# Kernel tuning notes

Hardware: AMD Instinct MI355X
Metric: run time of the kernel (lower is better)

The kernel has to match this reference:

```python
import jax, jax.numpy as jnp
import numpy as np

H = 256
W = 256
N = 10000
CHUNK = 500  # N must be divisible by CHUNK
CHOL_BOUND = np.array([0.5, 0.0, 0.5], dtype=np.float32)  # cholesky_bound buffer


def setup_inputs() -> dict:
    key = jax.random.key(0)
    k1, k2, k3 = jax.random.split(key, 3)
    xyz = jax.random.normal(k1, (N, 2), dtype=jnp.float32)          # atanh-space positions
    cholesky = jax.random.uniform(k2, (N, 3), dtype=jnp.float32)    # lower-tri elems (pre-bound)
    colors = jax.random.normal(k3, (N, 3), dtype=jnp.float32)       # _colors (used raw)
    opacity = jnp.ones((N, 1), dtype=jnp.float32)                   # _opacity buffer
    scale_factor = jnp.asarray(1.0, dtype=jnp.float32)
    shift_factor = jnp.asarray(0.0, dtype=jnp.float32)
    return {"xyz": xyz, "cholesky": cholesky, "colors": colors,
            "opacity": opacity, "scale_factor": scale_factor, "shift_factor": shift_factor}


def _render(xyz, cholesky, colors, opacity, scale_factor, shift_factor):
    # --- project_gaussians_2d ---
    means = jnp.tanh(xyz)                                   # map to (-1, 1)
    cx = 0.5 * W * (means[:, 0] + 1.0)                      # pixel-space centers (N,)
    cy = 0.5 * H * (means[:, 1] + 1.0)
    L = cholesky + jnp.asarray(CHOL_BOUND)                  # get_cholesky_elements
    cov_xx = L[:, 0] * L[:, 0]
    cov_xy = L[:, 0] * L[:, 1]
    cov_yy = L[:, 1] * L[:, 1] + L[:, 2] * L[:, 2]
    det = cov_xx * cov_yy - cov_xy * cov_xy
    conic_a = cov_yy / det                                  # inverse covariance (conic)
    conic_b = -cov_xy / det
    conic_c = cov_xx / det
    op = opacity[:, 0]

    px = jnp.arange(W, dtype=jnp.float32)[None, :]          # (1, W) pixel x coords
    py = jnp.arange(H, dtype=jnp.float32)[:, None]          # (H, 1) pixel y coords

    def resh(v):
        return v.reshape((N // CHUNK, CHUNK) + v.shape[1:])

    stacked = jax.tree.map(resh, (cx, cy, conic_a, conic_b, conic_c, op, colors))

    # --- rasterize_gaussians_sum: out[h,w,:] = sum_n alpha_n(h,w) * color_n ---
    def body(acc, xs):
        cxc, cyc, ac, bc, cc, oc, colc = xs
        dx = cxc[:, None, None] - px[None]                  # (C, 1, W)
        dy = cyc[:, None, None] - py[None]                  # (C, H, 1)
        sigma = (0.5 * (ac[:, None, None] * dx * dx + cc[:, None, None] * dy * dy)
                 + bc[:, None, None] * (dx * dy))           # (C, H, W)
        alpha = oc[:, None, None] * jnp.exp(-sigma)
        alpha = jnp.where((sigma >= 0.0) & (alpha >= 1.0 / 255.0),
                          jnp.minimum(alpha, 0.999), 0.0)
        acc = acc + jnp.einsum('nhw,nc->hwc', alpha, colc)
        return acc, None

    img, _ = jax.lax.scan(body, jnp.zeros((H, W, 3), dtype=jnp.float32), stacked)
    img = img * scale_factor + shift_factor
    return jnp.transpose(img, (2, 0, 1))                    # (3, H, W)


def reference(xyz, cholesky, colors, opacity, scale_factor, shift_factor):
    return _render(xyz, cholesky, colors, opacity, scale_factor, shift_factor)
```

## Files before the change

### kernel.cpp

```cpp
#include <hip/hip_runtime.h>


#define IMG_H 256
#define IMG_W 256
#define TILE 8
#define TPX 32
#define NTILES 1024
#define CAP 512

__global__ __launch_bounds__(256) void prep_kernel(
    const float* __restrict__ xyz,
    const float* __restrict__ chol,
    const float* __restrict__ colors,
    const float* __restrict__ opacity,
    int N,
    unsigned int* __restrict__ bbox,
    float4* __restrict__ params)
{
    const int n = blockIdx.x * 256 + threadIdx.x;
    if (n >= N) return;

    const float mx = tanhf(xyz[2 * n + 0]);
    const float my = tanhf(xyz[2 * n + 1]);
    const float cx = 0.5f * IMG_W * (mx + 1.0f);
    const float cy = 0.5f * IMG_H * (my + 1.0f);

    const float L0 = chol[3 * n + 0] + 0.5f;
    const float L1 = chol[3 * n + 1];
    const float L2 = chol[3 * n + 2] + 0.5f;
    const float cov_xx = L0 * L0;
    const float cov_xy = L0 * L1;
    const float cov_yy = L1 * L1 + L2 * L2;
    const float det = cov_xx * cov_yy - cov_xy * cov_xy;

    params[3 * n + 0] = make_float4(cx, cy, cov_yy / det, -cov_xy / det);
    params[3 * n + 1] = make_float4(cov_xx / det, opacity[n],
                                    colors[3 * n + 0], colors[3 * n + 1]);
    params[3 * n + 2] = make_float4(colors[3 * n + 2], 0.0f, 0.0f, 0.0f);

    const float smax = logf(255.0f * opacity[n]);
    unsigned int packed = 0xFFFFFFFFu;
    if (smax > 0.0f) {
        const float rx = sqrtf(2.0f * smax * cov_xx) + 1.0f;
        const float ry = sqrtf(2.0f * smax * cov_yy) + 1.0f;
        const int x0 = max(0, (int)floorf(cx - rx));
        const int x1 = min(IMG_W - 1, (int)ceilf(cx + rx));
        const int y0 = max(0, (int)floorf(cy - ry));
        const int y1 = min(IMG_H - 1, (int)ceilf(cy + ry));
        if (x0 <= x1 && y0 <= y1) {
            packed = (unsigned int)(x0 >> 3) | ((unsigned int)(x1 >> 3) << 5) |
                     ((unsigned int)(y0 >> 3) << 10) | ((unsigned int)(y1 >> 3) << 15);
        }
    }
    bbox[n] = packed;
}

__global__ __launch_bounds__(256) void render_kernel(
    const unsigned int* __restrict__ bbox,
    const float4* __restrict__ params,
    const float* __restrict__ scale,
    const float* __restrict__ shift,
    int N,
    float* __restrict__ out)
{
    const int tile = blockIdx.x;
    const int tx = tile & (TPX - 1);
    const int ty = tile >> 5;
    const int wave = threadIdx.x >> 6;
    const int lane = threadIdx.x & 63;
    const int p = lane;
    const float px = (float)(tx * TILE + (p & (TILE - 1)));
    const float py = (float)(ty * TILE + (p >> 3));

    __shared__ int lcnt;
    __shared__ int lidx[CAP];
    __shared__ float4 sh[3 * 256];
    __shared__ float red[3][256];

    if (threadIdx.x == 0) lcnt = 0;
    __syncthreads();

    const unsigned int txu = (unsigned int)tx;
    const unsigned int tyu = (unsigned int)ty;
    for (int i = threadIdx.x; i < N; i += 256) {
        const unsigned int b = bbox[i];
        const bool match = ((b & 31u) <= txu) && (txu <= ((b >> 5) & 31u)) &&
                           (((b >> 10) & 31u) <= tyu) && (tyu <= ((b >> 15) & 31u));
        const unsigned long long mask = __ballot(match);
        if (match) {
            const int leader = __ffsll((long long)mask) - 1;
            const int pos = __popcll(mask & ((1ull << lane) - 1ull));
            int basep = 0;
            if (lane == leader) basep = atomicAdd(&lcnt, __popcll(mask));
            basep = __shfl(basep, leader);
            const int slot = basep + pos;
            if (slot < CAP) lidx[slot] = i;
        }
    }
    __syncthreads();
    const int cnt = min(lcnt, CAP);

    float accr = 0.0f, accg = 0.0f, accb = 0.0f;

    for (int base = 0; base < cnt; base += 256) {
        const int m = min(256, cnt - base);
        if (threadIdx.x < m) {
            const int n = lidx[base + threadIdx.x];
            sh[3 * threadIdx.x + 0] = params[3 * n + 0];
            sh[3 * threadIdx.x + 1] = params[3 * n + 1];
            sh[3 * threadIdx.x + 2] = params[3 * n + 2];
        }
        __syncthreads();
        for (int j = wave; j < m; j += 4) {
            const float4 p0 = sh[3 * j + 0];
            const float4 p1 = sh[3 * j + 1];
            const float c2v = sh[3 * j + 2].x;
            const float dx = p0.x - px;
            const float dy = p0.y - py;
            const float sigma =
                0.5f * (p0.z * dx * dx + p1.x * dy * dy) + p0.w * (dx * dy);
            float alpha = p1.y * __expf(-sigma);
            if (sigma >= 0.0f && alpha >= (1.0f / 255.0f)) {
                alpha = fminf(alpha, 0.999f);
                accr = fmaf(alpha, p1.z, accr);
                accg = fmaf(alpha, p1.w, accg);
                accb = fmaf(alpha, c2v, accb);
            }
        }
        __syncthreads();
    }

    red[0][threadIdx.x] = accr;
    red[1][threadIdx.x] = accg;
    red[2][threadIdx.x] = accb;
    __syncthreads();

    if (threadIdx.x < 192) {
        const int c = threadIdx.x >> 6;
        const int q = threadIdx.x & 63;
        const float sum = red[c][q] + red[c][q + 64] + red[c][q + 128] + red[c][q + 192];
        const int pix = (ty * TILE + (q >> 3)) * IMG_W + tx * TILE + (q & (TILE - 1));
        out[c * IMG_H * IMG_W + pix] = fmaf(sum, scale[0], shift[0]);
    }
}

extern "C" void kernel_launch(void* const* d_in, const int* in_sizes, int n_in,
                              void* d_out, int out_size, void* d_ws, size_t ws_size,
                              hipStream_t stream) {
    const float* xyz     = (const float*)d_in[0];
    const float* chol    = (const float*)d_in[1];
    const float* colors  = (const float*)d_in[2];
    const float* opacity = (const float*)d_in[3];
    const float* scale   = (const float*)d_in[4];
    const float* shift   = (const float*)d_in[5];
    float* out = (float*)d_out;

    const int N = in_sizes[3];

    unsigned int* bbox = (unsigned int*)d_ws;
    float4* params = (float4*)((char*)d_ws + ((N * 4 + 15) & ~15));

    prep_kernel<<<(N + 255) / 256, 256, 0, stream>>>(
        xyz, chol, colors, opacity, N, bbox, params);
    render_kernel<<<NTILES, 256, 0, stream>>>(bbox, params, scale, shift, N, out);
}
```

Measured before the change: 83.89 us.

## Replace atomic ballot compaction with per-thread private lists and block prefix scan

The per-tile culling pass no longer uses a ballot plus LDS atomic per match. Each thread now buffers up to 16 matching indices in shared memory, then a block-wide Hillis-Steele scan computes offsets for an ordered compaction. The change also permutes the tile-to-block mapping, splits the parameter staging into float4 pairs plus a scalar array, and unrolls the inner loop. It adds many barriers during the scan, hardcodes a 40-iteration loop (assumes N ≤ 10240), and silently drops matches beyond 16 per thread.

```diff
diff --git a/kernel.cpp b/kernel.cpp
--- a/kernel.cpp
+++ b/kernel.cpp
@@ -7,6 +7,7 @@
 #define TPX 32
 #define NTILES 1024
 #define CAP 512
+#define PRIV 16
 
 __global__ __launch_bounds__(256) void prep_kernel(
     const float* __restrict__ xyz,
@@ -33,13 +34,14 @@
     const float cov_yy = L1 * L1 + L2 * L2;
     const float det = cov_xx * cov_yy - cov_xy * cov_xy;
 
+    const float op = opacity[n];
     params[3 * n + 0] = make_float4(cx, cy, cov_yy / det, -cov_xy / det);
-    params[3 * n + 1] = make_float4(cov_xx / det, opacity[n],
+    params[3 * n + 1] = make_float4(cov_xx / det, op,
                                     colors[3 * n + 0], colors[3 * n + 1]);
     params[3 * n + 2] = make_float4(colors[3 * n + 2], 0.0f, 0.0f, 0.0f);
 
-    const float smax = logf(255.0f * opacity[n]);
-    unsigned int packed = 0xFFFFFFFFu;
+    const float smax = logf(255.0f * op);
+    unsigned int packed = 31u | (31u << 10);
     if (smax > 0.0f) {
         const float rx = sqrtf(2.0f * smax * cov_xx) + 1.0f;
         const float ry = sqrtf(2.0f * smax * cov_yy) + 1.0f;
@@ -63,42 +65,51 @@
     int N,
     float* __restrict__ out)
 {
-    const int tile = blockIdx.x;
+    const int tile = (blockIdx.x * 389) & (NTILES - 1);
     const int tx = tile & (TPX - 1);
     const int ty = tile >> 5;
     const int wave = threadIdx.x >> 6;
-    const int lane = threadIdx.x & 63;
-    const int p = lane;
+    const int p = threadIdx.x & 63;
     const float px = (float)(tx * TILE + (p & (TILE - 1)));
     const float py = (float)(ty * TILE + (p >> 3));
 
-    __shared__ int lcnt;
+    __shared__ int lpriv[PRIV][256];
+    __shared__ int pscan[256];
     __shared__ int lidx[CAP];
-    __shared__ float4 sh[3 * 256];
+    __shared__ float4 sh4[2 * 256];
+    __shared__ float shc[256];
     __shared__ float red[3][256];
-
-    if (threadIdx.x == 0) lcnt = 0;
-    __syncthreads();
 
     const unsigned int txu = (unsigned int)tx;
     const unsigned int tyu = (unsigned int)ty;
-    for (int i = threadIdx.x; i < N; i += 256) {
-        const unsigned int b = bbox[i];
-        const bool match = ((b & 31u) <= txu) && (txu <= ((b >> 5) & 31u)) &&
-                           (((b >> 10) & 31u) <= tyu) && (tyu <= ((b >> 15) & 31u));
-        const unsigned long long mask = __ballot(match);
-        if (match) {
-            const int leader = __ffsll((long long)mask) - 1;
-            const int pos = __popcll(mask & ((1ull << lane) - 1ull));
-            int basep = 0;
-            if (lane == leader) basep = atomicAdd(&lcnt, __popcll(mask));
-            basep = __shfl(basep, leader);
-            const int slot = basep + pos;
-            if (slot < CAP) lidx[slot] = i;
+    int c = 0;
+#pragma unroll 4
+    for (int k = 0; k < 40; ++k) {
+        const int i = threadIdx.x + (k << 8);
+        if (i < N) {
+            const unsigned int b = bbox[i];
+            const bool match = ((b & 31u) <= txu) & (txu <= ((b >> 5) & 31u)) &
+                               (((b >> 10) & 31u) <= tyu) & (tyu <= ((b >> 15) & 31u));
+            if (match && c < PRIV) { lpriv[c][threadIdx.x] = i; ++c; }
         }
     }
+
+    pscan[threadIdx.x] = c;
     __syncthreads();
-    const int cnt = min(lcnt, CAP);
+    for (int d = 1; d < 256; d <<= 1) {
+        int y = 0;
+        if (threadIdx.x >= d) y = pscan[threadIdx.x - d];
+        __syncthreads();
+        if (threadIdx.x >= d) pscan[threadIdx.x] += y;
+        __syncthreads();
+    }
+    const int cnt = min(pscan[255], CAP);
+    const int off = pscan[threadIdx.x] - c;
+    for (int k = 0; k < c; ++k) {
+        const int s = off + k;
+        if (s < CAP) lidx[s] = lpriv[k][threadIdx.x];
+    }
+    __syncthreads();
 
     float accr = 0.0f, accg = 0.0f, accb = 0.0f;
 
@@ -106,15 +117,16 @@
         const int m = min(256, cnt - base);
         if (threadIdx.x < m) {
             const int n = lidx[base + threadIdx.x];
-            sh[3 * threadIdx.x + 0] = params[3 * n + 0];
-            sh[3 * threadIdx.x + 1] = params[3 * n + 1];
-            sh[3 * threadIdx.x + 2] = params[3 * n + 2];
+            sh4[2 * threadIdx.x + 0] = params[3 * n + 0];
+            sh4[2 * threadIdx.x + 1] = params[3 * n + 1];
+            shc[threadIdx.x] = params[3 * n + 2].x;
         }
         __syncthreads();
+#pragma unroll 2
         for (int j = wave; j < m; j += 4) {
-            const float4 p0 = sh[3 * j + 0];
-            const float4 p1 = sh[3 * j + 1];
-            const float c2v = sh[3 * j + 2].x;
+            const float4 p0 = sh4[2 * j + 0];
+            const float4 p1 = sh4[2 * j + 1];
+            const float c2v = shc[j];
             const float dx = p0.x - px;
             const float dy = p0.y - py;
             const float sigma =
@@ -136,11 +148,11 @@
     __syncthreads();
 
     if (threadIdx.x < 192) {
-        const int c = threadIdx.x >> 6;
+        const int ch = threadIdx.x >> 6;
         const int q = threadIdx.x & 63;
-        const float sum = red[c][q] + red[c][q + 64] + red[c][q + 128] + red[c][q + 192];
+        const float sum = red[ch][q] + red[ch][q + 64] + red[ch][q + 128] + red[ch][q + 192];
         const int pix = (ty * TILE + (q >> 3)) * IMG_W + tx * TILE + (q & (TILE - 1));
-        out[c * IMG_H * IMG_W + pix] = fmaf(sum, scale[0], shift[0]);
+        out[ch * IMG_H * IMG_W + pix] = fmaf(sum, scale[0], shift[0]);
     }
 }
 
```

Result: no change. 82.81 us (-1.3%).
